# Kernel optimization log

Hardware: AMD Instinct MI355X
Metric: run time of the kernel (lower is better)

The kernel has to match this reference:

```python
import jax, jax.numpy as jnp
import numpy as np
import math

B, S, H = 1, 2048, 2048
NH = 16            # num attention heads (== num kv heads -> group_factor 1)
NOPE, ROPE, DV = 128, 64, 128
DQK = NOPE + ROPE  # 192
QR, KVR = 768, 512 # q/kv lora ranks
E, K, M = 16, 4, 1024  # routed experts, topk, moe intermediate
SCALE = 2.5        # routed_scaling_factor
EPS = 1e-6
ROPE_BASE = 10000.0


def _rmsnorm(x, w, eps=EPS):
    var = jnp.mean(x * x, axis=-1, keepdims=True)
    return x * jax.lax.rsqrt(var + eps) * w


def _rotate_half(x):
    x1, x2 = jnp.split(x, 2, axis=-1)
    return jnp.concatenate([-x2, x1], axis=-1)


def _rope_tables(seqlen, dim, base=ROPE_BASE):
    inv_freq = 1.0 / (base ** (jnp.arange(0, dim, 2, dtype=jnp.float32) / dim))
    t = jnp.arange(seqlen, dtype=jnp.float32)
    freqs = t[:, None] * inv_freq[None, :]
    emb = jnp.concatenate([freqs, freqs], axis=-1)  # [S, dim]
    # broadcast over batch and heads: [1, S, 1, dim]
    return jnp.cos(emb)[None, :, None, :], jnp.sin(emb)[None, :, None, :]


def setup_inputs() -> dict:
    key = jax.random.key(0)
    ks = jax.random.split(key, 20)
    std = 0.02
    x = jax.random.normal(ks[0], (B, S, H), dtype=jnp.float32)
    causal = jnp.tril(jnp.ones((S, S), dtype=bool))
    attention_mask = jnp.where(causal, 0.0, -1e9).astype(jnp.float32)[None, None]
    p = lambda k, shape: jax.random.normal(k, shape, dtype=jnp.float32) * std
    return {
        "x": x,
        "attention_mask": attention_mask,
        "ln1_w": jnp.ones((H,), jnp.float32),
        "ln2_w": jnp.ones((H,), jnp.float32),
        "q_a_w": p(ks[1], (QR, H)),
        "q_a_ln": jnp.ones((QR,), jnp.float32),
        "q_b_w": p(ks[2], (NH * DQK, QR)),
        "kv_a_w": p(ks[3], (KVR, H)),
        "kv_a_ln": jnp.ones((KVR,), jnp.float32),
        "kv_b_w": p(ks[4], (NH * (DQK + DV), KVR)),
        "o_w": p(ks[5], (H, NH * DV)),
        "router_w": p(ks[6], (E, H)),
        "router_b": jnp.zeros((E,), jnp.float32),
        "gate_w": p(ks[7], (E, M, H)),
        "up_w": p(ks[8], (E, M, H)),
        "down_w": p(ks[9], (E, H, M)),
        "sg_w": p(ks[10], (M, H)),
        "su_w": p(ks[11], (M, H)),
        "sd_w": p(ks[12], (H, M)),
    }


def _attention(x, mask, q_a_w, q_a_ln, q_b_w, kv_a_w, kv_a_ln, kv_b_w, o_w):
    q = _rmsnorm(x @ q_a_w.T, q_a_ln)           # [B,S,QR]
    kv = _rmsnorm(x @ kv_a_w.T, kv_a_ln)        # [B,S,KVR]
    q = (q @ q_b_w.T).reshape(B, S, NH, DQK)
    kv = (kv @ kv_b_w.T).reshape(B, S, NH, DQK + DV)
    k_nope, k_rope, v = jnp.split(kv, [NOPE, NOPE + ROPE], axis=-1)
    q_nope, q_rope = jnp.split(q, [NOPE], axis=-1)
    cos, sin = _rope_tables(S, ROPE)
    q_rope = q_rope * cos + _rotate_half(q_rope) * sin
    k_rope = k_rope * cos + _rotate_half(k_rope) * sin
    qf = jnp.concatenate([q_nope, q_rope], axis=-1)   # [B,S,NH,DQK]
    kf = jnp.concatenate([k_nope, k_rope], axis=-1)
    scores = jnp.einsum("bqhd,bkhd->bhqk", qf, kf) / math.sqrt(DQK)
    scores = scores + mask
    attn = jax.nn.softmax(scores, axis=-1)
    ctx = jnp.einsum("bhqk,bkhd->bqhd", attn, v).reshape(B, S, NH * DV)
    return ctx @ o_w.T


def _moe(x, router_w, router_b, gate_w, up_w, down_w, sg_w, su_w, sd_w):
    T = B * S
    xf = x.reshape(T, H)
    logits = xf @ router_w.T + router_b            # [T,E]
    probs = jax.nn.sigmoid(logits)                 # scoring_func='sigmoid'
    topv, topi = jax.lax.top_k(probs, K)           # [T,K]
    w = topv / (jnp.sum(topv, axis=-1, keepdims=True) + 1e-9)  # norm_topk_prob
    w = w * SCALE
    rows = jnp.arange(T)[:, None]
    combine = jnp.zeros((T, E), xf.dtype).at[rows, topi].add(w)  # [T,E]
    # dense grouped-expert compute, masked combine (same math as gather/scatter loop)
    g = jnp.einsum("th,emh->tem", xf, gate_w)      # [T,E,M]
    u = jnp.einsum("th,emh->tem", xf, up_w)
    act = jax.nn.silu(g) * u
    routed = jnp.einsum("tem,ehm,te->th", act, down_w, combine)
    shared = (jax.nn.silu(xf @ sg_w.T) * (xf @ su_w.T)) @ sd_w.T
    return (routed + shared).reshape(B, S, H)


def reference(x, attention_mask, ln1_w, ln2_w, q_a_w, q_a_ln, q_b_w,
              kv_a_w, kv_a_ln, kv_b_w, o_w, router_w, router_b,
              gate_w, up_w, down_w, sg_w, su_w, sd_w):
    h1 = _rmsnorm(x, ln1_w)
    x = x + _attention(h1, attention_mask, q_a_w, q_a_ln, q_b_w,
                       kv_a_w, kv_a_ln, kv_b_w, o_w)
    h2 = _rmsnorm(x, ln2_w)
    x = x + _moe(h2, router_w, router_b, gate_w, up_w, down_w, sg_w, su_w, sd_w)
    return x
```

## Files before the change

### kernel.cpp

```cpp
#include <hip/hip_runtime.h>

typedef _Float16 f16x8 __attribute__((ext_vector_type(8)));
typedef float f32x4 __attribute__((ext_vector_type(4)));

__global__ __launch_bounds__(256) void rmsnorm_f32(const float* __restrict__ x,
                                                   const float* __restrict__ w,
                                                   float* __restrict__ out, int cols) {
    int row = blockIdx.x;
    const float* xr = x + (size_t)row * cols;
    float ss = 0.f;
    for (int c = threadIdx.x; c < cols; c += 256) { float v = xr[c]; ss += v * v; }
    __shared__ float red[256];
    red[threadIdx.x] = ss; __syncthreads();
    for (int s = 128; s > 0; s >>= 1) {
        if ((int)threadIdx.x < s) red[threadIdx.x] += red[threadIdx.x + s];
        __syncthreads();
    }
    float scale = rsqrtf(red[0] / (float)cols + 1e-6f);
    float* orow = out + (size_t)row * cols;
    for (int c = threadIdx.x; c < cols; c += 256) orow[c] = xr[c] * scale * w[c];
}

__global__ __launch_bounds__(256) void gemm_mfma_abt(const float* __restrict__ A,
                                                     const float* __restrict__ B,
                                                     float* __restrict__ C,
                                                     int N, int K,
                                                     const float* __restrict__ residual) {
    int bm = blockIdx.y * 128, bn = blockIdx.x * 128;
    __shared__ _Float16 Ash[128][40];
    __shared__ _Float16 Bsh[128][40];

    int tid = threadIdx.x;
    int srow = tid >> 1;
    int skoff = (tid & 1) * 16;
    const float* Aptr = A + (size_t)(bm + srow) * K + skoff;
    const float* Bptr = B + (size_t)(bn + srow) * K + skoff;

    float4 pa[4], pb[4];
    #pragma unroll
    for (int j = 0; j < 4; ++j) {
        pa[j] = *reinterpret_cast<const float4*>(Aptr + 4 * j);
        pb[j] = *reinterpret_cast<const float4*>(Bptr + 4 * j);
    }

    int wid = tid >> 6;
    int lane = tid & 63;
    int wr = (wid >> 1) * 64;
    int wc = (wid & 1) * 64;
    int fr = lane & 15;
    int fk = (lane >> 4) * 8;

    f32x4 acc[4][4];
    #pragma unroll
    for (int i = 0; i < 4; ++i)
        #pragma unroll
        for (int j = 0; j < 4; ++j) acc[i][j] = (f32x4)(0.f);

    int nsteps = K >> 5;
    for (int s = 0; s < nsteps; ++s) {
        __syncthreads();
        #pragma unroll
        for (int g = 0; g < 2; ++g) {
            float4 v0 = pa[2 * g], v1 = pa[2 * g + 1];
            f16x8 ha;
            ha[0] = (_Float16)v0.x; ha[1] = (_Float16)v0.y;
            ha[2] = (_Float16)v0.z; ha[3] = (_Float16)v0.w;
            ha[4] = (_Float16)v1.x; ha[5] = (_Float16)v1.y;
            ha[6] = (_Float16)v1.z; ha[7] = (_Float16)v1.w;
            *reinterpret_cast<f16x8*>(&Ash[srow][skoff + 8 * g]) = ha;
            float4 w0 = pb[2 * g], w1 = pb[2 * g + 1];
            f16x8 hb;
            hb[0] = (_Float16)w0.x; hb[1] = (_Float16)w0.y;
            hb[2] = (_Float16)w0.z; hb[3] = (_Float16)w0.w;
            hb[4] = (_Float16)w1.x; hb[5] = (_Float16)w1.y;
            hb[6] = (_Float16)w1.z; hb[7] = (_Float16)w1.w;
            *reinterpret_cast<f16x8*>(&Bsh[srow][skoff + 8 * g]) = hb;
        }
        __syncthreads();
        if (s + 1 < nsteps) {
            const float* ap = Aptr + (size_t)(s + 1) * 32;
            const float* bp = Bptr + (size_t)(s + 1) * 32;
            #pragma unroll
            for (int j = 0; j < 4; ++j) {
                pa[j] = *reinterpret_cast<const float4*>(ap + 4 * j);
                pb[j] = *reinterpret_cast<const float4*>(bp + 4 * j);
            }
        }
        f16x8 af[4], bf[4];
        #pragma unroll
        for (int i = 0; i < 4; ++i)
            af[i] = *reinterpret_cast<const f16x8*>(&Ash[wr + i * 16 + fr][fk]);
        #pragma unroll
        for (int j = 0; j < 4; ++j)
            bf[j] = *reinterpret_cast<const f16x8*>(&Bsh[wc + j * 16 + fr][fk]);
        #pragma unroll
        for (int i = 0; i < 4; ++i)
            #pragma unroll
            for (int j = 0; j < 4; ++j)
                acc[i][j] = __builtin_amdgcn_mfma_f32_16x16x32_f16(af[i], bf[j], acc[i][j], 0, 0, 0);
    }

    int crow = (lane >> 4) * 4;
    int ccol = lane & 15;
    #pragma unroll
    for (int i = 0; i < 4; ++i) {
        #pragma unroll
        for (int ii = 0; ii < 4; ++ii) {
            size_t m = bm + wr + i * 16 + crow + ii;
            float* cp = C + m * N + bn + wc + ccol;
            if (residual) {
                const float* rp = residual + m * N + bn + wc + ccol;
                #pragma unroll
                for (int j = 0; j < 4; ++j) cp[j * 16] = acc[i][j][ii] + rp[j * 16];
            } else {
                #pragma unroll
                for (int j = 0; j < 4; ++j) cp[j * 16] = acc[i][j][ii];
            }
        }
    }
}

__global__ __launch_bounds__(256) void rope_kernel(float* __restrict__ qfull, float* __restrict__ kvfull, int T) {
    int idx = blockIdx.x * 256 + threadIdx.x;
    int total = T * 16 * 32;
    if (idx >= total) return;
    int i = idx & 31;
    int h = (idx >> 5) & 15;
    int t = idx >> 9;
    float invf = powf(10000.0f, -(float)(2 * i) / 64.0f);
    float ang = (float)t * invf;
    float c = cosf(ang), s = sinf(ang);
    float* qr = qfull + (size_t)t * 3072 + h * 192 + 128;
    float x1 = qr[i], x2 = qr[i + 32];
    qr[i] = x1 * c - x2 * s;
    qr[i + 32] = x2 * c + x1 * s;
    float* kr = kvfull + (size_t)t * 5120 + h * 320 + 128;
    x1 = kr[i]; x2 = kr[i + 32];
    kr[i] = x1 * c - x2 * s;
    kr[i + 32] = x2 * c + x1 * s;
}

__global__ __launch_bounds__(256, 2) void attn_mfma(const float* __restrict__ qfull,
                                                    const float* __restrict__ kvfull,
                                                    float* __restrict__ ctx) {
    __shared__ _Float16 Qs[64][200];
    __shared__ _Float16 Ks[64][200];
    __shared__ _Float16 Vst[128][72];
    __shared__ _Float16 Ps[64][72];

    int bid = blockIdx.x;
    int h = bid & 15;
    int i = bid >> 4;
    int qt = (i < 16) ? i : 47 - i;
    int q0 = qt * 64;
    int tid = threadIdx.x;

    {
        int row = tid >> 2;
        int cb = (tid & 3) * 48;
        const float* qp = qfull + (size_t)(q0 + row) * 3072 + h * 192 + cb;
        #pragma unroll
        for (int m = 0; m < 6; ++m) {
            float4 v0 = *reinterpret_cast<const float4*>(qp + 8 * m);
            float4 v1 = *reinterpret_cast<const float4*>(qp + 8 * m + 4);
            f16x8 hv;
            hv[0] = (_Float16)v0.x; hv[1] = (_Float16)v0.y;
            hv[2] = (_Float16)v0.z; hv[3] = (_Float16)v0.w;
            hv[4] = (_Float16)v1.x; hv[5] = (_Float16)v1.y;
            hv[6] = (_Float16)v1.z; hv[7] = (_Float16)v1.w;
            *reinterpret_cast<f16x8*>(&Qs[row][cb + 8 * m]) = hv;
        }
    }

    int wid = tid >> 6;
    int lane = tid & 63;
    int wrow0 = wid * 16;
    int fr = lane & 15;
    int g = lane >> 4;
    int fk8 = g * 8;

    f32x4 acc_o[8];
    #pragma unroll
    for (int n = 0; n < 8; ++n) acc_o[n] = (f32x4)(0.f);
    float mrun[4] = {-3e38f, -3e38f, -3e38f, -3e38f};
    float lrun[4] = {0.f, 0.f, 0.f, 0.f};

    const float scale = 0.07216878364870322f;
    int vd = tid & 127;
    int vn0 = tid >> 7;
    int nchunk = qt + 1;

    for (int ci = 0; ci < nchunk; ++ci) {
        int k0 = ci * 64;
        __syncthreads();
        {
            int row = tid >> 2;
            int cb = (tid & 3) * 48;
            const float* kp = kvfull + (size_t)(k0 + row) * 5120 + h * 320 + cb;
            #pragma unroll
            for (int m = 0; m < 6; ++m) {
                float4 v0 = *reinterpret_cast<const float4*>(kp + 8 * m);
                float4 v1 = *reinterpret_cast<const float4*>(kp + 8 * m + 4);
                f16x8 hv;
                hv[0] = (_Float16)v0.x; hv[1] = (_Float16)v0.y;
                hv[2] = (_Float16)v0.z; hv[3] = (_Float16)v0.w;
                hv[4] = (_Float16)v1.x; hv[5] = (_Float16)v1.y;
                hv[6] = (_Float16)v1.z; hv[7] = (_Float16)v1.w;
                *reinterpret_cast<f16x8*>(&Ks[row][cb + 8 * m]) = hv;
            }
        }
        {
            const float* vp = kvfull + (size_t)(k0 + vn0) * 5120 + h * 320 + 192 + vd;
            #pragma unroll
            for (int j = 0; j < 32; ++j)
                Vst[vd][vn0 + 2 * j] = (_Float16)vp[(size_t)10240 * j];
        }
        __syncthreads();

        f32x4 accs[4];
        #pragma unroll
        for (int j = 0; j < 4; ++j) accs[j] = (f32x4)(0.f);
        #pragma unroll
        for (int s = 0; s < 6; ++s) {
            f16x8 a = *reinterpret_cast<const f16x8*>(&Qs[wrow0 + fr][32 * s + fk8]);
            #pragma unroll
            for (int j = 0; j < 4; ++j) {
                f16x8 b = *reinterpret_cast<const f16x8*>(&Ks[16 * j + fr][32 * s + fk8]);
                accs[j] = __builtin_amdgcn_mfma_f32_16x16x32_f16(a, b, accs[j], 0, 0, 0);
            }
        }

        bool diag = (k0 == q0);
        float p[4][4];
        #pragma unroll
        for (int reg = 0; reg < 4; ++reg) {
            int grow = wrow0 + 4 * g + reg;
            float sv[4];
            #pragma unroll
            for (int j = 0; j < 4; ++j) {
                float v = accs[j][reg] * scale;
                sv[j] = (diag && (16 * j + fr > grow)) ? -3e38f : v;
            }
            float rm = fmaxf(fmaxf(sv[0], sv[1]), fmaxf(sv[2], sv[3]));
            rm = fmaxf(rm, __shfl_xor(rm, 1));
            rm = fmaxf(rm, __shfl_xor(rm, 2));
            rm = fmaxf(rm, __shfl_xor(rm, 4));
            rm = fmaxf(rm, __shfl_xor(rm, 8));
            float mn = fmaxf(mrun[reg], rm);
            float co = __expf(mrun[reg] - mn);
            mrun[reg] = mn;
            float rs = 0.f;
            #pragma unroll
            for (int j = 0; j < 4; ++j) {
                float pv = __expf(sv[j] - mn);
                p[reg][j] = pv; rs += pv;
            }
            rs += __shfl_xor(rs, 1);
            rs += __shfl_xor(rs, 2);
            rs += __shfl_xor(rs, 4);
            rs += __shfl_xor(rs, 8);
            lrun[reg] = lrun[reg] * co + rs;
            #pragma unroll
            for (int n = 0; n < 8; ++n) acc_o[n][reg] *= co;
        }

        #pragma unroll
        for (int reg = 0; reg < 4; ++reg)
            #pragma unroll
            for (int j = 0; j < 4; ++j)
                Ps[wrow0 + 4 * g + reg][16 * j + fr] = (_Float16)p[reg][j];

        #pragma unroll
        for (int s = 0; s < 2; ++s) {
            f16x8 a = *reinterpret_cast<const f16x8*>(&Ps[wrow0 + fr][32 * s + fk8]);
            #pragma unroll
            for (int n = 0; n < 8; ++n) {
                f16x8 b = *reinterpret_cast<const f16x8*>(&Vst[16 * n + fr][32 * s + fk8]);
                acc_o[n] = __builtin_amdgcn_mfma_f32_16x16x32_f16(a, b, acc_o[n], 0, 0, 0);
            }
        }
    }

    float inv[4];
    #pragma unroll
    for (int reg = 0; reg < 4; ++reg) inv[reg] = 1.0f / lrun[reg];
    #pragma unroll
    for (int reg = 0; reg < 4; ++reg) {
        float* op = ctx + (size_t)(q0 + wrow0 + 4 * g + reg) * 2048 + h * 128 + fr;
        #pragma unroll
        for (int n = 0; n < 8; ++n) op[16 * n] = acc_o[n][reg] * inv[reg];
    }
}

__global__ __launch_bounds__(256) void router_kernel(const float* __restrict__ h2,
                                                     const float* __restrict__ rw,
                                                     const float* __restrict__ rb,
                                                     int* __restrict__ topi, float* __restrict__ topw) {
    int t = blockIdx.x;
    int tid = threadIdx.x;
    int e = tid >> 4;
    int lane = tid & 15;
    const float* xr = h2 + (size_t)t * 2048;
    const float* wr = rw + (size_t)e * 2048;
    float partial = 0.f;
    for (int hh = lane; hh < 2048; hh += 16) partial += xr[hh] * wr[hh];
    __shared__ float red[256];
    __shared__ float probs[16];
    red[tid] = partial; __syncthreads();
    for (int s = 8; s > 0; s >>= 1) {
        if (lane < s) red[tid] += red[tid + s];
        __syncthreads();
    }
    if (lane == 0) {
        float logit = red[tid] + rb[e];
        probs[e] = 1.0f / (1.0f + __expf(-logit));
    }
    __syncthreads();
    if (tid == 0) {
        bool used[16] = {false};
        int idxs[4]; float vals[4]; float sum = 0.f;
        for (int k = 0; k < 4; ++k) {
            float best = -1e30f; int bi = 0;
            for (int ee = 0; ee < 16; ++ee)
                if (!used[ee] && probs[ee] > best) { best = probs[ee]; bi = ee; }
            used[bi] = true; idxs[k] = bi; vals[k] = best; sum += best;
        }
        float invs = 2.5f / (sum + 1e-9f);
        for (int k = 0; k < 4; ++k) { topi[t * 4 + k] = idxs[k]; topw[t * 4 + k] = vals[k] * invs; }
    }
}

__global__ __launch_bounds__(256) void moe_bucket(const int* __restrict__ topi,
                                                  const float* __restrict__ topw,
                                                  int* __restrict__ btok, float* __restrict__ bw,
                                                  int* __restrict__ gcnt, int* __restrict__ goff,
                                                  int* __restrict__ pidx) {
    __shared__ int cnt[16], off[16], cur[16];
    int tid = threadIdx.x;
    if (tid < 16) { cnt[tid] = 0; cur[tid] = 0; }
    __syncthreads();
    for (int p = tid; p < 8192; p += 256) atomicAdd(&cnt[topi[p]], 1);
    __syncthreads();
    if (tid == 0) { int s = 0; for (int e = 0; e < 16; ++e) { off[e] = s; s += cnt[e]; } }
    __syncthreads();
    for (int p = tid; p < 8192; p += 256) {
        int e = topi[p];
        int pos = off[e] + atomicAdd(&cur[e], 1);
        btok[pos] = p >> 2;
        bw[pos] = topw[p];
        pidx[p] = pos;
    }
    if (tid < 16) { gcnt[tid] = cnt[tid]; goff[tid] = off[tid]; }
}

__global__ __launch_bounds__(256) void moe_gemm_mfma(const float* __restrict__ A,
                                                     const float* __restrict__ W,
                                                     float* __restrict__ Cf,
                                                     _Float16* __restrict__ Ch,
                                                     const int* __restrict__ btok,
                                                     const int* __restrict__ cnt,
                                                     const int* __restrict__ off,
                                                     int N, int K, int mode) {
    int e = blockIdx.z;
    int ce = cnt[e];
    int r0 = blockIdx.y * 128;
    if (r0 >= ce) return;
    int oe = off[e];
    int bn = blockIdx.x * 128;

    __shared__ _Float16 Ash[128][40];
    __shared__ _Float16 Bsh[128][40];

    int tid = threadIdx.x;
    int srow = tid >> 1;
    int skoff = (tid & 1) * 16;

    int arow = r0 + srow;
    int arow_c = (arow < ce) ? arow : (ce - 1);
    const float* Aptr;
    if (mode == 0) Aptr = A + (size_t)btok[oe + arow_c] * K + skoff;
    else           Aptr = A + (size_t)(oe + arow_c) * K + skoff;
    const float* Bptr = W + (size_t)e * N * K + (size_t)(bn + srow) * K + skoff;

    float4 pa[4], pb[4];
    #pragma unroll
    for (int j = 0; j < 4; ++j) {
        pa[j] = *reinterpret_cast<const float4*>(Aptr + 4 * j);
        pb[j] = *reinterpret_cast<const float4*>(Bptr + 4 * j);
    }

    int wid = tid >> 6;
    int lane = tid & 63;
    int wr = (wid >> 1) * 64;
    int wc = (wid & 1) * 64;
    int fr = lane & 15;
    int fk = (lane >> 4) * 8;

    f32x4 acc[4][4];
    #pragma unroll
    for (int i = 0; i < 4; ++i)
        #pragma unroll
        for (int j = 0; j < 4; ++j) acc[i][j] = (f32x4)(0.f);

    int nsteps = K >> 5;
    for (int s = 0; s < nsteps; ++s) {
        __syncthreads();
        #pragma unroll
        for (int g = 0; g < 2; ++g) {
            float4 v0 = pa[2 * g], v1 = pa[2 * g + 1];
            f16x8 ha;
            ha[0] = (_Float16)v0.x; ha[1] = (_Float16)v0.y;
            ha[2] = (_Float16)v0.z; ha[3] = (_Float16)v0.w;
            ha[4] = (_Float16)v1.x; ha[5] = (_Float16)v1.y;
            ha[6] = (_Float16)v1.z; ha[7] = (_Float16)v1.w;
            *reinterpret_cast<f16x8*>(&Ash[srow][skoff + 8 * g]) = ha;
            float4 w0 = pb[2 * g], w1 = pb[2 * g + 1];
            f16x8 hb;
            hb[0] = (_Float16)w0.x; hb[1] = (_Float16)w0.y;
            hb[2] = (_Float16)w0.z; hb[3] = (_Float16)w0.w;
            hb[4] = (_Float16)w1.x; hb[5] = (_Float16)w1.y;
            hb[6] = (_Float16)w1.z; hb[7] = (_Float16)w1.w;
            *reinterpret_cast<f16x8*>(&Bsh[srow][skoff + 8 * g]) = hb;
        }
        __syncthreads();
        if (s + 1 < nsteps) {
            const float* ap = Aptr + (size_t)(s + 1) * 32;
            const float* bp = Bptr + (size_t)(s + 1) * 32;
            #pragma unroll
            for (int j = 0; j < 4; ++j) {
                pa[j] = *reinterpret_cast<const float4*>(ap + 4 * j);
                pb[j] = *reinterpret_cast<const float4*>(bp + 4 * j);
            }
        }
        f16x8 af[4], bf[4];
        #pragma unroll
        for (int i = 0; i < 4; ++i)
            af[i] = *reinterpret_cast<const f16x8*>(&Ash[wr + i * 16 + fr][fk]);
        #pragma unroll
        for (int j = 0; j < 4; ++j)
            bf[j] = *reinterpret_cast<const f16x8*>(&Bsh[wc + j * 16 + fr][fk]);
        #pragma unroll
        for (int i = 0; i < 4; ++i)
            #pragma unroll
            for (int j = 0; j < 4; ++j)
                acc[i][j] = __builtin_amdgcn_mfma_f32_16x16x32_f16(af[i], bf[j], acc[i][j], 0, 0, 0);
    }

    int crow = (lane >> 4) * 4;
    int ccol = lane & 15;
    #pragma unroll
    for (int i = 0; i < 4; ++i) {
        #pragma unroll
        for (int ii = 0; ii < 4; ++ii) {
            int ri = r0 + wr + i * 16 + crow + ii;
            if (ri < ce) {
                if (mode == 0) {
                    float* cp = Cf + (size_t)(oe + ri) * N + bn + wc + ccol;
                    #pragma unroll
                    for (int j = 0; j < 4; ++j) cp[j * 16] = acc[i][j][ii];
                } else {
                    _Float16* cp = Ch + (size_t)(oe + ri) * N + bn + wc + ccol;
                    #pragma unroll
                    for (int j = 0; j < 4; ++j) cp[j * 16] = (_Float16)acc[i][j][ii];
                }
            }
        }
    }
}

__global__ __launch_bounds__(256) void moe_combine(float* __restrict__ out,
                                                   const _Float16* __restrict__ part,
                                                   const int* __restrict__ pidx) {
    int t = blockIdx.x;
    int c8 = threadIdx.x * 8;
    float* op = out + (size_t)t * 2048 + c8;
    float acc[8];
    *reinterpret_cast<float4*>(&acc[0]) = *reinterpret_cast<const float4*>(op);
    *reinterpret_cast<float4*>(&acc[4]) = *reinterpret_cast<const float4*>(op + 4);
    #pragma unroll
    for (int k = 0; k < 4; ++k) {
        const f16x8 pv = *reinterpret_cast<const f16x8*>(part + (size_t)pidx[t * 4 + k] * 2048 + c8);
        #pragma unroll
        for (int j = 0; j < 8; ++j) acc[j] += (float)pv[j];
    }
    *reinterpret_cast<float4*>(op) = *reinterpret_cast<float4*>(&acc[0]);
    *reinterpret_cast<float4*>(op + 4) = *reinterpret_cast<float4*>(&acc[4]);
}

__global__ __launch_bounds__(256) void act_silu(float* __restrict__ g, const float* __restrict__ u,
                                                const float* __restrict__ bw, int n) {
    int i = blockIdx.x * 256 + threadIdx.x;
    if (i < n) {
        float gv = g[i];
        float s = gv / (1.0f + __expf(-gv));
        g[i] = bw[i >> 10] * s * u[i];
    }
}

__global__ __launch_bounds__(256) void silu_mul(const float* __restrict__ g, const float* __restrict__ u,
                                                float* __restrict__ o, int n) {
    int i = blockIdx.x * 256 + threadIdx.x;
    if (i < n) { float gv = g[i]; o[i] = gv / (1.0f + __expf(-gv)) * u[i]; }
}

extern "C" void kernel_launch(void* const* d_in, const int* in_sizes, int n_in,
                              void* d_out, int out_size, void* d_ws, size_t ws_size,
                              hipStream_t stream) {
    (void)in_sizes; (void)n_in; (void)out_size; (void)ws_size;
    const float* x        = (const float*)d_in[0];
    const float* ln1_w    = (const float*)d_in[2];
    const float* ln2_w    = (const float*)d_in[3];
    const float* q_a_w    = (const float*)d_in[4];
    const float* q_a_ln   = (const float*)d_in[5];
    const float* q_b_w    = (const float*)d_in[6];
    const float* kv_a_w   = (const float*)d_in[7];
    const float* kv_a_ln  = (const float*)d_in[8];
    const float* kv_b_w   = (const float*)d_in[9];
    const float* o_w      = (const float*)d_in[10];
    const float* router_w = (const float*)d_in[11];
    const float* router_b = (const float*)d_in[12];
    const float* gate_w   = (const float*)d_in[13];
    const float* up_w     = (const float*)d_in[14];
    const float* down_w   = (const float*)d_in[15];
    const float* sg_w     = (const float*)d_in[16];
    const float* su_w     = (const float*)d_in[17];
    const float* sd_w     = (const float*)d_in[18];

    const size_t T = 2048;
    float* ws = (float*)d_ws;
    float* x2  = ws;
    float* h2  = x2 + 4194304;
    float* big = h2 + 4194304;
    float* h1     = big;
    float* qa     = h1 + 4194304;
    float* kva    = qa + 1572864;
    float* qfull  = kva + 1048576;
    float* kvfull = qfull + 6291456;
    float* ctxb   = h1;
    float* g = big;
    float* u = big + 8388608;
    _Float16* part = (_Float16*)u;
    int*   topi = (int*)(big + 16777216);
    float* topw = (float*)(topi + 8192);
    int*   btok = (int*)(topw + 8192);
    float* bw   = (float*)(btok + 8192);
    int*   cntg = (int*)(bw + 8192);
    int*   offg = cntg + 16;
    int*   pidx = offg + 16;
    float* sg   = big + 16777216 + 65536;
    float* su   = sg + 2097152;
    float* ash  = su + 2097152;

    rmsnorm_f32<<<T, 256, 0, stream>>>(x, ln1_w, h1, 2048);
    gemm_mfma_abt<<<dim3(768 / 128, T / 128), 256, 0, stream>>>(h1, q_a_w, qa, 768, 2048, nullptr);
    gemm_mfma_abt<<<dim3(512 / 128, T / 128), 256, 0, stream>>>(h1, kv_a_w, kva, 512, 2048, nullptr);
    rmsnorm_f32<<<T, 256, 0, stream>>>(qa, q_a_ln, qa, 768);
    rmsnorm_f32<<<T, 256, 0, stream>>>(kva, kv_a_ln, kva, 512);
    gemm_mfma_abt<<<dim3(3072 / 128, T / 128), 256, 0, stream>>>(qa, q_b_w, qfull, 3072, 768, nullptr);
    gemm_mfma_abt<<<dim3(5120 / 128, T / 128), 256, 0, stream>>>(kva, kv_b_w, kvfull, 5120, 512, nullptr);
    rope_kernel<<<(T * 16 * 32) / 256, 256, 0, stream>>>(qfull, kvfull, (int)T);
    attn_mfma<<<512, 256, 0, stream>>>(qfull, kvfull, ctxb);
    gemm_mfma_abt<<<dim3(2048 / 128, T / 128), 256, 0, stream>>>(ctxb, o_w, x2, 2048, 2048, x);
    rmsnorm_f32<<<T, 256, 0, stream>>>(x2, ln2_w, h2, 2048);
    router_kernel<<<T, 256, 0, stream>>>(h2, router_w, router_b, topi, topw);
    moe_bucket<<<1, 256, 0, stream>>>(topi, topw, btok, bw, cntg, offg, pidx);
    moe_gemm_mfma<<<dim3(8, 16, 16), 256, 0, stream>>>(h2, gate_w, g, nullptr, btok, cntg, offg, 1024, 2048, 0);
    moe_gemm_mfma<<<dim3(8, 16, 16), 256, 0, stream>>>(h2, up_w, u, nullptr, btok, cntg, offg, 1024, 2048, 0);
    act_silu<<<(8192 * 1024) / 256, 256, 0, stream>>>(g, u, bw, 8192 * 1024);
    moe_gemm_mfma<<<dim3(16, 16, 16), 256, 0, stream>>>(g, down_w, nullptr, part, btok, cntg, offg, 2048, 1024, 1);
    gemm_mfma_abt<<<dim3(1024 / 128, T / 128), 256, 0, stream>>>(h2, sg_w, sg, 1024, 2048, nullptr);
    gemm_mfma_abt<<<dim3(1024 / 128, T / 128), 256, 0, stream>>>(h2, su_w, su, 1024, 2048, nullptr);
    silu_mul<<<(T * 1024) / 256, 256, 0, stream>>>(sg, su, ash, (int)(T * 1024));
    gemm_mfma_abt<<<dim3(2048 / 128, T / 128), 256, 0, stream>>>(ash, sd_w, (float*)d_out, 2048, 1024, x2);
    moe_combine<<<2048, 256, 0, stream>>>((float*)d_out, part, pidx);
}
```

Measured before the change: 1.452 ms.

## Fuse SiLU-gating into MoE up GEMM, fp16 intermediate, XCD-aware block remap

The routed-expert SiLU·up·weight step moves into the epilogue of the up-projection GEMM, which reads the gate result and writes an fp16 activation buffer. This drops the separate act_silu pass and the fp32 up buffer. The down GEMM now loads fp16 activations directly, halving its A-operand traffic. Block indices are also remapped so that consecutive blocks go to the same XCD, aiming for better L2 reuse, though this changes the order blocks are scheduled in.

After: 1.382 ms. -4.8%, faster.

```diff
diff --git a/kernel.cpp b/kernel.cpp
--- a/kernel.cpp
+++ b/kernel.cpp
@@ -353,20 +353,30 @@
     if (tid < 16) { gcnt[tid] = cnt[tid]; goff[tid] = off[tid]; }
 }
 
-__global__ __launch_bounds__(256) void moe_gemm_mfma(const float* __restrict__ A,
+__device__ inline void xcd_remap(int NX, int NY, int& bx, int& by, int& e) {
+    int R = blockIdx.x + NX * (blockIdx.y + NY * blockIdx.z);
+    int total = NX * NY * gridDim.z;
+    int L = (R & 7) * (total >> 3) + (R >> 3);
+    bx = L % NX;
+    int t2 = L / NX;
+    by = t2 % NY;
+    e = t2 / NY;
+}
+
+__global__ __launch_bounds__(256) void moe_gemm_gate(const float* __restrict__ A,
                                                      const float* __restrict__ W,
                                                      float* __restrict__ Cf,
-                                                     _Float16* __restrict__ Ch,
                                                      const int* __restrict__ btok,
                                                      const int* __restrict__ cnt,
                                                      const int* __restrict__ off,
-                                                     int N, int K, int mode) {
-    int e = blockIdx.z;
+                                                     int N, int K) {
+    int bx, by, e;
+    xcd_remap(gridDim.x, gridDim.y, bx, by, e);
     int ce = cnt[e];
-    int r0 = blockIdx.y * 128;
+    int r0 = by * 128;
     if (r0 >= ce) return;
     int oe = off[e];
-    int bn = blockIdx.x * 128;
+    int bn = bx * 128;
 
     __shared__ _Float16 Ash[128][40];
     __shared__ _Float16 Bsh[128][40];
@@ -377,9 +387,7 @@
 
     int arow = r0 + srow;
     int arow_c = (arow < ce) ? arow : (ce - 1);
-    const float* Aptr;
-    if (mode == 0) Aptr = A + (size_t)btok[oe + arow_c] * K + skoff;
-    else           Aptr = A + (size_t)(oe + arow_c) * K + skoff;
+    const float* Aptr = A + (size_t)btok[oe + arow_c] * K + skoff;
     const float* Bptr = W + (size_t)e * N * K + (size_t)(bn + srow) * K + skoff;
 
     float4 pa[4], pb[4];
@@ -454,15 +462,227 @@
         for (int ii = 0; ii < 4; ++ii) {
             int ri = r0 + wr + i * 16 + crow + ii;
             if (ri < ce) {
-                if (mode == 0) {
-                    float* cp = Cf + (size_t)(oe + ri) * N + bn + wc + ccol;
-                    #pragma unroll
-                    for (int j = 0; j < 4; ++j) cp[j * 16] = acc[i][j][ii];
-                } else {
-                    _Float16* cp = Ch + (size_t)(oe + ri) * N + bn + wc + ccol;
-                    #pragma unroll
-                    for (int j = 0; j < 4; ++j) cp[j * 16] = (_Float16)acc[i][j][ii];
+                float* cp = Cf + (size_t)(oe + ri) * N + bn + wc + ccol;
+                #pragma unroll
+                for (int j = 0; j < 4; ++j) cp[j * 16] = acc[i][j][ii];
+            }
+        }
+    }
+}
+
+__global__ __launch_bounds__(256) void moe_gemm_up(const float* __restrict__ A,
+                                                   const float* __restrict__ W,
+                                                   const float* __restrict__ gbuf,
+                                                   const float* __restrict__ bwp,
+                                                   _Float16* __restrict__ act,
+                                                   const int* __restrict__ btok,
+                                                   const int* __restrict__ cnt,
+                                                   const int* __restrict__ off,
+                                                   int N, int K) {
+    int bx, by, e;
+    xcd_remap(gridDim.x, gridDim.y, bx, by, e);
+    int ce = cnt[e];
+    int r0 = by * 128;
+    if (r0 >= ce) return;
+    int oe = off[e];
+    int bn = bx * 128;
+
+    __shared__ _Float16 Ash[128][40];
+    __shared__ _Float16 Bsh[128][40];
+
+    int tid = threadIdx.x;
+    int srow = tid >> 1;
+    int skoff = (tid & 1) * 16;
+
+    int arow = r0 + srow;
+    int arow_c = (arow < ce) ? arow : (ce - 1);
+    const float* Aptr = A + (size_t)btok[oe + arow_c] * K + skoff;
+    const float* Bptr = W + (size_t)e * N * K + (size_t)(bn + srow) * K + skoff;
+
+    float4 pa[4], pb[4];
+    #pragma unroll
+    for (int j = 0; j < 4; ++j) {
+        pa[j] = *reinterpret_cast<const float4*>(Aptr + 4 * j);
+        pb[j] = *reinterpret_cast<const float4*>(Bptr + 4 * j);
+    }
+
+    int wid = tid >> 6;
+    int lane = tid & 63;
+    int wr = (wid >> 1) * 64;
+    int wc = (wid & 1) * 64;
+    int fr = lane & 15;
+    int fk = (lane >> 4) * 8;
+
+    f32x4 acc[4][4];
+    #pragma unroll
+    for (int i = 0; i < 4; ++i)
+        #pragma unroll
+        for (int j = 0; j < 4; ++j) acc[i][j] = (f32x4)(0.f);
+
+    int nsteps = K >> 5;
+    for (int s = 0; s < nsteps; ++s) {
+        __syncthreads();
+        #pragma unroll
+        for (int g = 0; g < 2; ++g) {
+            float4 v0 = pa[2 * g], v1 = pa[2 * g + 1];
+            f16x8 ha;
+            ha[0] = (_Float16)v0.x; ha[1] = (_Float16)v0.y;
+            ha[2] = (_Float16)v0.z; ha[3] = (_Float16)v0.w;
+            ha[4] = (_Float16)v1.x; ha[5] = (_Float16)v1.y;
+            ha[6] = (_Float16)v1.z; ha[7] = (_Float16)v1.w;
+            *reinterpret_cast<f16x8*>(&Ash[srow][skoff + 8 * g]) = ha;
+            float4 w0 = pb[2 * g], w1 = pb[2 * g + 1];
+            f16x8 hb;
+            hb[0] = (_Float16)w0.x; hb[1] = (_Float16)w0.y;
+            hb[2] = (_Float16)w0.z; hb[3] = (_Float16)w0.w;
+            hb[4] = (_Float16)w1.x; hb[5] = (_Float16)w1.y;
+            hb[6] = (_Float16)w1.z; hb[7] = (_Float16)w1.w;
+            *reinterpret_cast<f16x8*>(&Bsh[srow][skoff + 8 * g]) = hb;
+        }
+        __syncthreads();
+        if (s + 1 < nsteps) {
+            const float* ap = Aptr + (size_t)(s + 1) * 32;
+            const float* bp = Bptr + (size_t)(s + 1) * 32;
+            #pragma unroll
+            for (int j = 0; j < 4; ++j) {
+                pa[j] = *reinterpret_cast<const float4*>(ap + 4 * j);
+                pb[j] = *reinterpret_cast<const float4*>(bp + 4 * j);
+            }
+        }
+        f16x8 af[4], bf[4];
+        #pragma unroll
+        for (int i = 0; i < 4; ++i)
+            af[i] = *reinterpret_cast<const f16x8*>(&Ash[wr + i * 16 + fr][fk]);
+        #pragma unroll
+        for (int j = 0; j < 4; ++j)
+            bf[j] = *reinterpret_cast<const f16x8*>(&Bsh[wc + j * 16 + fr][fk]);
+        #pragma unroll
+        for (int i = 0; i < 4; ++i)
+            #pragma unroll
+            for (int j = 0; j < 4; ++j)
+                acc[i][j] = __builtin_amdgcn_mfma_f32_16x16x32_f16(af[i], bf[j], acc[i][j], 0, 0, 0);
+    }
+
+    int crow = (lane >> 4) * 4;
+    int ccol = lane & 15;
+    #pragma unroll
+    for (int i = 0; i < 4; ++i) {
+        #pragma unroll
+        for (int ii = 0; ii < 4; ++ii) {
+            int ri = r0 + wr + i * 16 + crow + ii;
+            if (ri < ce) {
+                int p = oe + ri;
+                float w = bwp[p];
+                const float* gp = gbuf + (size_t)p * N + bn + wc + ccol;
+                _Float16* ap = act + (size_t)p * N + bn + wc + ccol;
+                #pragma unroll
+                for (int j = 0; j < 4; ++j) {
+                    float gv = gp[j * 16];
+                    float sv = gv / (1.0f + __expf(-gv));
+                    ap[j * 16] = (_Float16)(w * sv * acc[i][j][ii]);
                 }
+            }
+        }
+    }
+}
+
+__global__ __launch_bounds__(256) void moe_gemm_down16(const _Float16* __restrict__ A,
+                                                       const float* __restrict__ W,
+                                                       _Float16* __restrict__ Ch,
+                                                       const int* __restrict__ cnt,
+                                                       const int* __restrict__ off,
+                                                       int N, int K) {
+    int bx, by, e;
+    xcd_remap(gridDim.x, gridDim.y, bx, by, e);
+    int ce = cnt[e];
+    int r0 = by * 128;
+    if (r0 >= ce) return;
+    int oe = off[e];
+    int bn = bx * 128;
+
+    __shared__ _Float16 Ash[128][40];
+    __shared__ _Float16 Bsh[128][40];
+
+    int tid = threadIdx.x;
+    int srow = tid >> 1;
+    int skoff = (tid & 1) * 16;
+
+    int arow = r0 + srow;
+    int arow_c = (arow < ce) ? arow : (ce - 1);
+    const _Float16* Aptr = A + (size_t)(oe + arow_c) * K + skoff;
+    const float* Bptr = W + (size_t)e * N * K + (size_t)(bn + srow) * K + skoff;
+
+    f16x8 pah[2];
+    float4 pb[4];
+    pah[0] = *reinterpret_cast<const f16x8*>(Aptr);
+    pah[1] = *reinterpret_cast<const f16x8*>(Aptr + 8);
+    #pragma unroll
+    for (int j = 0; j < 4; ++j)
+        pb[j] = *reinterpret_cast<const float4*>(Bptr + 4 * j);
+
+    int wid = tid >> 6;
+    int lane = tid & 63;
+    int wr = (wid >> 1) * 64;
+    int wc = (wid & 1) * 64;
+    int fr = lane & 15;
+    int fk = (lane >> 4) * 8;
+
+    f32x4 acc[4][4];
+    #pragma unroll
+    for (int i = 0; i < 4; ++i)
+        #pragma unroll
+        for (int j = 0; j < 4; ++j) acc[i][j] = (f32x4)(0.f);
+
+    int nsteps = K >> 5;
+    for (int s = 0; s < nsteps; ++s) {
+        __syncthreads();
+        *reinterpret_cast<f16x8*>(&Ash[srow][skoff]) = pah[0];
+        *reinterpret_cast<f16x8*>(&Ash[srow][skoff + 8]) = pah[1];
+        #pragma unroll
+        for (int g = 0; g < 2; ++g) {
+            float4 w0 = pb[2 * g], w1 = pb[2 * g + 1];
+            f16x8 hb;
+            hb[0] = (_Float16)w0.x; hb[1] = (_Float16)w0.y;
+            hb[2] = (_Float16)w0.z; hb[3] = (_Float16)w0.w;
+            hb[4] = (_Float16)w1.x; hb[5] = (_Float16)w1.y;
+            hb[6] = (_Float16)w1.z; hb[7] = (_Float16)w1.w;
+            *reinterpret_cast<f16x8*>(&Bsh[srow][skoff + 8 * g]) = hb;
+        }
+        __syncthreads();
+        if (s + 1 < nsteps) {
+            const _Float16* ap = Aptr + (size_t)(s + 1) * 32;
+            const float* bp = Bptr + (size_t)(s + 1) * 32;
+            pah[0] = *reinterpret_cast<const f16x8*>(ap);
+            pah[1] = *reinterpret_cast<const f16x8*>(ap + 8);
+            #pragma unroll
+            for (int j = 0; j < 4; ++j)
+                pb[j] = *reinterpret_cast<const float4*>(bp + 4 * j);
+        }
+        f16x8 af[4], bf[4];
+        #pragma unroll
+        for (int i = 0; i < 4; ++i)
+            af[i] = *reinterpret_cast<const f16x8*>(&Ash[wr + i * 16 + fr][fk]);
+        #pragma unroll
+        for (int j = 0; j < 4; ++j)
+            bf[j] = *reinterpret_cast<const f16x8*>(&Bsh[wc + j * 16 + fr][fk]);
+        #pragma unroll
+        for (int i = 0; i < 4; ++i)
+            #pragma unroll
+            for (int j = 0; j < 4; ++j)
+                acc[i][j] = __builtin_amdgcn_mfma_f32_16x16x32_f16(af[i], bf[j], acc[i][j], 0, 0, 0);
+    }
+
+    int crow = (lane >> 4) * 4;
+    int ccol = lane & 15;
+    #pragma unroll
+    for (int i = 0; i < 4; ++i) {
+        #pragma unroll
+        for (int ii = 0; ii < 4; ++ii) {
+            int ri = r0 + wr + i * 16 + crow + ii;
+            if (ri < ce) {
+                _Float16* cp = Ch + (size_t)(oe + ri) * N + bn + wc + ccol;
+                #pragma unroll
+                for (int j = 0; j < 4; ++j) cp[j * 16] = (_Float16)acc[i][j][ii];
             }
         }
     }
@@ -485,16 +705,6 @@
     }
     *reinterpret_cast<float4*>(op) = *reinterpret_cast<float4*>(&acc[0]);
     *reinterpret_cast<float4*>(op + 4) = *reinterpret_cast<float4*>(&acc[4]);
-}
-
-__global__ __launch_bounds__(256) void act_silu(float* __restrict__ g, const float* __restrict__ u,
-                                                const float* __restrict__ bw, int n) {
-    int i = blockIdx.x * 256 + threadIdx.x;
-    if (i < n) {
-        float gv = g[i];
-        float s = gv / (1.0f + __expf(-gv));
-        g[i] = bw[i >> 10] * s * u[i];
-    }
 }
 
 __global__ __launch_bounds__(256) void silu_mul(const float* __restrict__ g, const float* __restrict__ u,
@@ -537,19 +747,19 @@
     float* qfull  = kva + 1048576;
     float* kvfull = qfull + 6291456;
     float* ctxb   = h1;
-    float* g = big;
-    float* u = big + 8388608;
-    _Float16* part = (_Float16*)u;
-    int*   topi = (int*)(big + 16777216);
+    float* g        = big;
+    _Float16* act   = (_Float16*)(big + 8388608);
+    _Float16* part  = (_Float16*)(big + 12582912);
+    int*   topi = (int*)(big + 20971520);
     float* topw = (float*)(topi + 8192);
     int*   btok = (int*)(topw + 8192);
-    float* bw   = (float*)(btok + 8192);
-    int*   cntg = (int*)(bw + 8192);
+    float* bwp  = (float*)(btok + 8192);
+    int*   cntg = (int*)(bwp + 8192);
     int*   offg = cntg + 16;
     int*   pidx = offg + 16;
-    float* sg   = big + 16777216 + 65536;
-    float* su   = sg + 2097152;
-    float* ash  = su + 2097152;
+    float* sg   = big;
+    float* su   = big + 2097152;
+    float* ash  = big + 4194304;
 
     rmsnorm_f32<<<T, 256, 0, stream>>>(x, ln1_w, h1, 2048);
     gemm_mfma_abt<<<dim3(768 / 128, T / 128), 256, 0, stream>>>(h1, q_a_w, qa, 768, 2048, nullptr);
@@ -563,11 +773,10 @@
     gemm_mfma_abt<<<dim3(2048 / 128, T / 128), 256, 0, stream>>>(ctxb, o_w, x2, 2048, 2048, x);
     rmsnorm_f32<<<T, 256, 0, stream>>>(x2, ln2_w, h2, 2048);
     router_kernel<<<T, 256, 0, stream>>>(h2, router_w, router_b, topi, topw);
-    moe_bucket<<<1, 256, 0, stream>>>(topi, topw, btok, bw, cntg, offg, pidx);
-    moe_gemm_mfma<<<dim3(8, 16, 16), 256, 0, stream>>>(h2, gate_w, g, nullptr, btok, cntg, offg, 1024, 2048, 0);
-    moe_gemm_mfma<<<dim3(8, 16, 16), 256, 0, stream>>>(h2, up_w, u, nullptr, btok, cntg, offg, 1024, 2048, 0);
-    act_silu<<<(8192 * 1024) / 256, 256, 0, stream>>>(g, u, bw, 8192 * 1024);
-    moe_gemm_mfma<<<dim3(16, 16, 16), 256, 0, stream>>>(g, down_w, nullptr, part, btok, cntg, offg, 2048, 1024, 1);
+    moe_bucket<<<1, 256, 0, stream>>>(topi, topw, btok, bwp, cntg, offg, pidx);
+    moe_gemm_gate<<<dim3(8, 16, 16), 256, 0, stream>>>(h2, gate_w, g, btok, cntg, offg, 1024, 2048);
+    moe_gemm_up<<<dim3(8, 16, 16), 256, 0, stream>>>(h2, up_w, g, bwp, act, btok, cntg, offg, 1024, 2048);
+    moe_gemm_down16<<<dim3(16, 16, 16), 256, 0, stream>>>(act, down_w, part, cntg, offg, 2048, 1024);
     gemm_mfma_abt<<<dim3(1024 / 128, T / 128), 256, 0, stream>>>(h2, sg_w, sg, 1024, 2048, nullptr);
     gemm_mfma_abt<<<dim3(1024 / 128, T / 128), 256, 0, stream>>>(h2, su_w, su, 1024, 2048, nullptr);
     silu_mul<<<(T * 1024) / 256, 256, 0, stream>>>(sg, su, ash, (int)(T * 1024));
```
